# Kernel optimization log

Hardware: AMD Instinct MI355X
Metric: run time of the kernel (lower is better)

The kernel has to match this reference:

```python
import jax, jax.numpy as jnp
import numpy as np
from jax import lax

CLAMP = 4.135
OUT = 7            # RoI pool output size
SCALE = 1.0 / 16.0 # feature-map stride 16


def bilinear_gather(feat, bidx, y, x):
    """feat [B,C,H,W]; bidx [N] int; y,x [N,Ph,Pw] coords in feature space -> [N,C,Ph,Pw]."""
    B, C, H, W = feat.shape
    y = jnp.clip(y, 0.0, H - 1.0)
    x = jnp.clip(x, 0.0, W - 1.0)
    y0 = jnp.floor(y); x0 = jnp.floor(x)
    y0i = y0.astype(jnp.int32); x0i = x0.astype(jnp.int32)
    y1i = jnp.minimum(y0i + 1, H - 1); x1i = jnp.minimum(x0i + 1, W - 1)
    wy1 = y - y0; wx1 = x - x0
    wy0 = 1.0 - wy1; wx0 = 1.0 - wx1
    flat = feat.transpose(0, 2, 3, 1).reshape(B * H * W, C)
    base = (bidx * (H * W))[:, None, None]
    def g(yy, xx):
        return flat[base + yy * W + xx]  # [N,Ph,Pw,C]
    out = ((wy0 * wx0)[..., None] * g(y0i, x0i)
           + (wy0 * wx1)[..., None] * g(y0i, x1i)
           + (wy1 * wx0)[..., None] * g(y1i, x0i)
           + (wy1 * wx1)[..., None] * g(y1i, x1i))
    return out.transpose(0, 3, 1, 2)


def roi_align(feat, boxes, bidx):
    """RoIAlign, sampling_ratio=1 (one bilinear sample per bin center)."""
    N = boxes.shape[0]
    b = boxes * SCALE
    x1, y1, x2, y2 = b[:, 0], b[:, 1], b[:, 2], b[:, 3]
    bw = jnp.maximum(x2 - x1, 1.0) / OUT
    bh = jnp.maximum(y2 - y1, 1.0) / OUT
    c = jnp.arange(OUT, dtype=feat.dtype) + 0.5
    ys = y1[:, None] + c * bh[:, None]   # [N,OUT]
    xs = x1[:, None] + c * bw[:, None]
    yg = jnp.broadcast_to(ys[:, :, None], (N, OUT, OUT))
    xg = jnp.broadcast_to(xs[:, None, :], (N, OUT, OUT))
    return bilinear_gather(feat, bidx, yg, xg)


def xyxy_to_rbox(b):
    cx = (b[:, 0] + b[:, 2]) * 0.5
    cy = (b[:, 1] + b[:, 3]) * 0.5
    w = b[:, 2] - b[:, 0]
    h = b[:, 3] - b[:, 1]
    return jnp.stack([cx, cy, w, h, jnp.zeros_like(cx)], axis=1)


def decode_deltas_to_rboxes(rboxes, deltas):
    cx, cy, w, h, a = (rboxes[:, i] for i in range(5))
    dx, dy, dw, dh, da = (deltas[:, i] for i in range(5))
    return jnp.stack([cx + dx * w, cy + dy * h,
                      w * jnp.exp(dw), h * jnp.exp(dh), a + da], axis=1)


def grid_sample_zeros(feat, gx, gy):
    """F.grid_sample(bilinear, padding_mode='zeros', align_corners=False).
    feat [N,C,H,W]; gx,gy [N,Ho,Wo] normalized coords -> [N,C,Ho,Wo]."""
    N, C, H, W = feat.shape
    ix = ((gx + 1.0) * W - 1.0) * 0.5
    iy = ((gy + 1.0) * H - 1.0) * 0.5
    x0 = jnp.floor(ix); y0 = jnp.floor(iy)
    wx1 = ix - x0; wy1 = iy - y0
    x0i = x0.astype(jnp.int32); y0i = y0.astype(jnp.int32)
    flat = feat.transpose(0, 2, 3, 1).reshape(N, H * W, C)
    Ho, Wo = gx.shape[1], gx.shape[2]
    def g(yy, xx, wt):
        valid = ((yy >= 0) & (yy < H) & (xx >= 0) & (xx < W)).astype(feat.dtype)
        idx = jnp.clip(yy, 0, H - 1) * W + jnp.clip(xx, 0, W - 1)
        v = jnp.take_along_axis(flat, idx.reshape(N, -1, 1), axis=1)
        v = v.reshape(N, Ho, Wo, C)
        return (wt * valid)[..., None] * v
    out = (g(y0i, x0i, (1 - wy1) * (1 - wx1))
           + g(y0i, x0i + 1, (1 - wy1) * wx1)
           + g(y0i + 1, x0i, wy1 * (1 - wx1))
           + g(y0i + 1, x0i + 1, wy1 * wx1))
    return out.transpose(0, 3, 1, 2)


def setup_inputs() -> dict:
    key = jax.random.key(0)
    ks = jax.random.split(key, 12)
    B, C, H, W = 2, 256, 64, 64
    N, NC = 2048, 16
    FD = C * OUT * OUT  # 12544
    features = jax.random.normal(ks[0], (B, C, H, W), jnp.float32)
    # valid image-space boxes (image 1024x1024, stride-16 features)
    cx = jax.random.uniform(ks[1], (N,), minval=96.0, maxval=928.0)
    cy = jax.random.uniform(ks[2], (N,), minval=96.0, maxval=928.0)
    bw = jax.random.uniform(ks[3], (N,), minval=16.0, maxval=128.0)
    bh = jax.random.uniform(ks[4], (N,), minval=16.0, maxval=128.0)
    proposals = jnp.stack([cx - bw / 2, cy - bh / 2, cx + bw / 2, cy + bh / 2], axis=1)
    batch_idx = jnp.repeat(jnp.arange(B, dtype=jnp.int32), N // B)
    s = 0.02
    return {
        "features": features,
        "proposals": proposals,
        "batch_idx": batch_idx,
        "conv_w": jax.random.normal(ks[5], (C, C, 3, 3), jnp.float32) * s,
        "conv_b": jnp.zeros((C,), jnp.float32),
        "align_w": jax.random.normal(ks[6], (5, FD), jnp.float32) * s,
        "align_b": jnp.zeros((5,), jnp.float32),
        "fc1_w": jax.random.normal(ks[7], (1024, FD), jnp.float32) * s,
        "fc1_b": jnp.zeros((1024,), jnp.float32),
        "fc2_w": jax.random.normal(ks[8], (1024, 1024), jnp.float32) * s,
        "fc2_b": jnp.zeros((1024,), jnp.float32),
        "cls_w": jax.random.normal(ks[9], (NC, 1024), jnp.float32) * s,
        "cls_b": jnp.zeros((NC,), jnp.float32),
        "box_w": jax.random.normal(ks[10], (5, 1024), jnp.float32) * s,
        "box_b": jnp.zeros((5,), jnp.float32),
    }


def reference(features, proposals, batch_idx, conv_w, conv_b, align_w, align_b,
              fc1_w, fc1_b, fc2_w, fc2_b, cls_w, cls_b, box_w, box_b):
    N = proposals.shape[0]
    # 1) RoI align
    box_feat = roi_align(features, proposals, batch_idx)           # [N,256,7,7]
    a = lax.conv_general_dilated(box_feat, conv_w, (1, 1), ((1, 1), (1, 1)),
                                 dimension_numbers=("NCHW", "OIHW", "NCHW"))
    a = jax.nn.relu(a + conv_b[None, :, None, None]).reshape(N, -1)
    coarse = jnp.clip(a @ align_w.T + align_b, -CLAMP, CLAMP)      # [N,5]
    # 3) decode to rboxes (torch.no_grad -> stop_gradient)
    prop_rb = xyxy_to_rbox(proposals)
    align_rb = lax.stop_gradient(decode_deltas_to_rboxes(prop_rb, coarse))
    # 4) affine grid from rbox (no translation, matches source) + grid_sample
    w, h, ang = align_rb[:, 2], align_rb[:, 3], align_rb[:, 4]
    cth, sth = jnp.cos(ang), jnp.sin(ang)
    sx, sy = w / OUT, h / OUT
    base = (2.0 * jnp.arange(OUT, dtype=box_feat.dtype) + 1.0) / OUT - 1.0
    xb = base[None, None, :]
    yb = base[None, :, None]
    gx = (sx * cth)[:, None, None] * xb + (-(sy * sth))[:, None, None] * yb
    gy = (sx * sth)[:, None, None] * xb + (sy * cth)[:, None, None] * yb
    aligned = grid_sample_zeros(box_feat, gx, gy)                  # [N,256,7,7]
    # 5) refine head MLP + predictors
    r = jax.nn.relu(aligned.reshape(N, -1) @ fc1_w.T + fc1_b)
    r = jax.nn.relu(r @ fc2_w.T + fc2_b)
    logits = r @ cls_w.T + cls_b                                   # [N,16]
    final = jnp.clip(r @ box_w.T + box_b, -CLAMP, CLAMP)           # [N,5]
    # 6) eval-path decode + softmax (per-class NMS is dynamic-shape postproc, excluded)
    pred_rboxes = decode_deltas_to_rboxes(prop_rb, final)
    scores = jax.nn.softmax(logits, axis=-1)
    return jnp.concatenate([pred_rboxes, scores], axis=1)          # [N,21]
```

## Files before the change

kernel.cpp:

```cpp
#include <hip/hip_runtime.h>
#include <hip/hip_bf16.h>
#include <math.h>
#include <type_traits>

constexpr int B = 2, C = 256, H = 64, W = 64, HW = H * W;
constexpr int N = 2048, OUT = 7, P = 49, FD = C * P;
constexpr int K1 = 1024;
constexpr float CLAMP_V = 4.135f, SCALE_V = 1.0f / 16.0f;
constexpr int LDB = 264;

typedef short s8v __attribute__((ext_vector_type(8)));
typedef short s4v __attribute__((ext_vector_type(4)));
typedef float f32x4 __attribute__((ext_vector_type(4)));

template <int I, int NN, class F>
__device__ __forceinline__ void static_for(F&& f) {
    if constexpr (I < NN) {
        f(std::integral_constant<int, I>{});
        static_for<I + 1, NN>(static_cast<F&&>(f));
    }
}

__device__ __forceinline__ int xcd_swz(int blk, int nblk) {
    const int cpx = nblk >> 3;
    return (blk & 7) * cpx + (blk >> 3);
}

__global__ void k_transpose_feat(const float* __restrict__ in, float* __restrict__ out) {
    __shared__ float tile[32][33];
    const int b  = blockIdx.z;
    const int c0 = blockIdx.y * 32;
    const int p0 = blockIdx.x * 32;
    const int tx = threadIdx.x % 32, ty = threadIdx.x / 32;
#pragma unroll
    for (int r = 0; r < 32; r += 8)
        tile[ty + r][tx] = in[(size_t)(b * C + c0 + ty + r) * HW + p0 + tx];
    __syncthreads();
#pragma unroll
    for (int r = 0; r < 32; r += 8)
        out[(size_t)(b * HW + p0 + ty + r) * C + c0 + tx] = tile[tx][ty + r];
}

__global__ void k_prep_wB(const float* __restrict__ in, __hip_bfloat16* __restrict__ out) {
    const int T = blockIdx.x;
    const int tap = T / 8, s = T % 8;
    const int co = threadIdx.x;
#pragma unroll
    for (int q = 0; q < 4; ++q)
#pragma unroll
        for (int j = 0; j < 8; ++j) {
            const int ci = s * 32 + q * 8 + j;
            out[(((size_t)T * 256 + co) * 4 + q) * 8 + j] =
                __float2bfloat16(in[(size_t)co * 2304 + ci * 9 + tap]);
        }
}

__global__ void k_prep_aw(const float* __restrict__ in, float4* __restrict__ out4,
                          float* __restrict__ out1) {
    const int o = blockIdx.x;
    const int co = threadIdx.x;
    float4 v;
    v.x = in[(size_t)0 * FD + co * 49 + o];
    v.y = in[(size_t)1 * FD + co * 49 + o];
    v.z = in[(size_t)2 * FD + co * 49 + o];
    v.w = in[(size_t)3 * FD + co * 49 + o];
    out4[o * 256 + co] = v;
    out1[o * 256 + co] = in[(size_t)4 * FD + co * 49 + o];
}

__global__ void k_f2b(const float* __restrict__ in, __hip_bfloat16* __restrict__ out, int n4) {
    for (int i = blockIdx.x * blockDim.x + threadIdx.x; i < n4; i += gridDim.x * blockDim.x) {
        const float4 v = reinterpret_cast<const float4*>(in)[i];
        out[i * 4 + 0] = __float2bfloat16(v.x);
        out[i * 4 + 1] = __float2bfloat16(v.y);
        out[i * 4 + 2] = __float2bfloat16(v.z);
        out[i * 4 + 3] = __float2bfloat16(v.w);
    }
}

__global__ void k_prep_fc1(const float* __restrict__ in, __hip_bfloat16* __restrict__ out) {
    __shared__ float lds[64 * 49];
    const int o  = blockIdx.y;
    const int c0 = blockIdx.x * 64;
    const int t  = threadIdx.x;
    const float* src = in + (size_t)o * FD + (size_t)c0 * 49;
    for (int i = t; i < 64 * 49; i += 256) lds[i] = src[i];
    __syncthreads();
    __hip_bfloat16* dst = out + (size_t)o * FD + c0;
    for (int j = t; j < 64 * 49; j += 256) {
        const int p = j >> 6, cc = j & 63;
        dst[(size_t)p * 256 + cc] = __float2bfloat16(lds[cc * 49 + p]);
    }
}

__global__ __launch_bounds__(256, 2) void k_roi_conv_grid(
    const float* __restrict__ featT, const float* __restrict__ proposals,
    const int* __restrict__ bidx, const __hip_bfloat16* __restrict__ wB,
    const float* __restrict__ conv_b, const float4* __restrict__ aw4,
    const float* __restrict__ aw1, const float* __restrict__ align_b,
    __hip_bfloat16* __restrict__ alignedOut) {
    __shared__ __align__(16) __hip_bfloat16 bfh[2][50 * LDB];
    __shared__ float red[64];

    const int blk = xcd_swz(blockIdx.x, 1024);
    const int t = threadIdx.x;
    const int lane = t & 63, wid = t >> 6;
    const int l15 = lane & 15;
    const int qofs = (lane >> 4) * 8;

#pragma unroll
    for (int r = 0; r < 2; ++r) {
        const int n = blk * 2 + r;
        const float px1 = proposals[n * 4 + 0] * SCALE_V, py1 = proposals[n * 4 + 1] * SCALE_V;
        const float px2 = proposals[n * 4 + 2] * SCALE_V, py2 = proposals[n * 4 + 3] * SCALE_V;
        const float bw = fmaxf(px2 - px1, 1.0f) * (1.0f / OUT);
        const float bh = fmaxf(py2 - py1, 1.0f) * (1.0f / OUT);
        const int b = bidx[n];
        const float* fb = featT + (size_t)b * HW * C;
        for (int p = wid; p < P; p += 4) {
            const int pyi = p / 7, pxi = p % 7;
            float y = py1 + (pyi + 0.5f) * bh;
            float x = px1 + (pxi + 0.5f) * bw;
            y = fminf(fmaxf(y, 0.f), (float)(H - 1));
            x = fminf(fmaxf(x, 0.f), (float)(W - 1));
            const float y0f = floorf(y), x0f = floorf(x);
            const int y0 = (int)y0f, x0 = (int)x0f;
            const int y1 = min(y0 + 1, H - 1), x1 = min(x0 + 1, W - 1);
            const float wy1 = y - y0f, wx1 = x - x0f;
            const float wy0 = 1.f - wy1, wx0 = 1.f - wx1;
            const int c4 = lane * 4;
            const float4 v00 = *reinterpret_cast<const float4*>(&fb[(size_t)(y0 * W + x0) * C + c4]);
            const float4 v01 = *reinterpret_cast<const float4*>(&fb[(size_t)(y0 * W + x1) * C + c4]);
            const float4 v10 = *reinterpret_cast<const float4*>(&fb[(size_t)(y1 * W + x0) * C + c4]);
            const float4 v11 = *reinterpret_cast<const float4*>(&fb[(size_t)(y1 * W + x1) * C + c4]);
            s4v o4;
            o4[0] = (short)__bfloat16_as_ushort(__float2bfloat16(
                        wy0 * (wx0 * v00.x + wx1 * v01.x) + wy1 * (wx0 * v10.x + wx1 * v11.x)));
            o4[1] = (short)__bfloat16_as_ushort(__float2bfloat16(
                        wy0 * (wx0 * v00.y + wx1 * v01.y) + wy1 * (wx0 * v10.y + wx1 * v11.y)));
            o4[2] = (short)__bfloat16_as_ushort(__float2bfloat16(
                        wy0 * (wx0 * v00.z + wx1 * v01.z) + wy1 * (wx0 * v10.z + wx1 * v11.z)));
            o4[3] = (short)__bfloat16_as_ushort(__float2bfloat16(
                        wy0 * (wx0 * v00.w + wx1 * v01.w) + wy1 * (wx0 * v10.w + wx1 * v11.w)));
            *reinterpret_cast<s4v*>(&bfh[r][p * LDB + c4]) = o4;
        }
        bfh[r][49 * LDB + t] = __float2bfloat16(0.f);
    }
    __syncthreads();

    int oyt[4], oxt[4];
    static_for<0, 4>([&](auto MT) {
        const int o = MT.value * 16 + l15;
        oyt[MT.value] = o / 7;
        oxt[MT.value] = o % 7;
    });
    int bofs[4];
    static_for<0, 4>([&](auto NT) {
        const int col = wid * 64 + NT.value * 16 + l15;
        bofs[NT.value] = col * 32 + qofs;
    });

    f32x4 acc[2][4][4] = {};
    for (int tap = 0; tap < 9; ++tap) {
        const int dy = tap / 3 - 1, dx = tap % 3 - 1;
        int rsel[4];
        static_for<0, 4>([&](auto MT) {
            const int iy = oyt[MT.value] + dy, ix = oxt[MT.value] + dx;
            const bool v = ((unsigned)iy < 7u) && ((unsigned)ix < 7u);
            rsel[MT.value] = (v ? (iy * 7 + ix) : 49) * LDB;
        });
        const __hip_bfloat16* wTap = wB + (size_t)tap * 8 * 8192;
#pragma unroll
        for (int s = 0; s < 8; ++s) {
            s8v af[2][4], bfr[4];
            static_for<0, 4>([&](auto NT) {
                bfr[NT.value] = *reinterpret_cast<const s8v*>(&wTap[(size_t)s * 8192 + bofs[NT.value]]);
            });
            static_for<0, 2>([&](auto RI) {
                static_for<0, 4>([&](auto MT) {
                    af[RI.value][MT.value] = *reinterpret_cast<const s8v*>(
                        &bfh[RI.value][rsel[MT.value] + s * 32 + qofs]);
                });
            });
            __builtin_amdgcn_s_setprio(1);
            static_for<0, 2>([&](auto RI) {
                static_for<0, 4>([&](auto MT) {
                    static_for<0, 4>([&](auto NT) {
                        acc[RI.value][MT.value][NT.value] = __builtin_amdgcn_mfma_f32_16x16x32_bf16(
                            af[RI.value][MT.value], bfr[NT.value],
                            acc[RI.value][MT.value][NT.value], 0, 0, 0);
                    });
                });
            });
            __builtin_amdgcn_s_setprio(0);
        }
    }

    float cb[4];
    static_for<0, 4>([&](auto NT) { cb[NT.value] = conv_b[wid * 64 + NT.value * 16 + l15]; });
    float pc[2][5] = {};
    static_for<0, 4>([&](auto MT) {
        static_for<0, 4>([&](auto RR) {
            const int o = MT.value * 16 + (lane >> 4) * 4 + RR.value;
            if (o < 49) {
                static_for<0, 4>([&](auto NT) {
                    const int co = wid * 64 + NT.value * 16 + l15;
                    const float4 w4 = aw4[o * 256 + co];
                    const float  w1 = aw1[o * 256 + co];
                    static_for<0, 2>([&](auto RI) {
                        const float a = fmaxf(acc[RI.value][MT.value][NT.value][RR.value] + cb[NT.value], 0.f);
                        pc[RI.value][0] = fmaf(a, w4.x, pc[RI.value][0]);
                        pc[RI.value][1] = fmaf(a, w4.y, pc[RI.value][1]);
                        pc[RI.value][2] = fmaf(a, w4.z, pc[RI.value][2]);
                        pc[RI.value][3] = fmaf(a, w4.w, pc[RI.value][3]);
                        pc[RI.value][4] = fmaf(a, w1,   pc[RI.value][4]);
                    });
                });
            }
        });
    });
    static_for<0, 2>([&](auto RI) {
        static_for<0, 5>([&](auto J) {
            float s = pc[RI.value][J.value];
#pragma unroll
            for (int off = 32; off; off >>= 1) s += __shfl_xor(s, off);
            pc[RI.value][J.value] = s;
        });
        if (lane == 0) {
            static_for<0, 5>([&](auto J) { red[RI.value * 20 + wid * 5 + J.value] = pc[RI.value][J.value]; });
        }
    });
    __syncthreads();

    if (t < 2) {
        const int r = t;
        const int n = blk * 2 + r;
        float coarse[5];
        static_for<0, 5>([&](auto Jc) {
            constexpr int j = Jc.value;
            float s = red[r * 20 + j] + red[r * 20 + 5 + j] + red[r * 20 + 10 + j] +
                      red[r * 20 + 15 + j] + align_b[j];
            coarse[j] = fminf(fmaxf(s, -CLAMP_V), CLAMP_V);
        });
        const float x1r = proposals[n * 4 + 0], y1r = proposals[n * 4 + 1];
        const float x2r = proposals[n * 4 + 2], y2r = proposals[n * 4 + 3];
        const float w = x2r - x1r, h = y2r - y1r;
        const float w2 = w * expf(coarse[2]);
        const float h2 = h * expf(coarse[3]);
        const float ang = coarse[4];
        const float cth = cosf(ang), sth = sinf(ang);
        const float sx = w2 * (1.0f / OUT), sy = h2 * (1.0f / OUT);
        red[48 + r * 4 + 0] = sx * cth;
        red[48 + r * 4 + 1] = sy * sth;
        red[48 + r * 4 + 2] = sx * sth;
        red[48 + r * 4 + 3] = sy * cth;
    }
    __syncthreads();

#pragma unroll
    for (int r = 0; r < 2; ++r) {
        const float gA = red[48 + r * 4 + 0], gBv = red[48 + r * 4 + 1];
        const float gC = red[48 + r * 4 + 2], gD = red[48 + r * 4 + 3];
        const __hip_bfloat16* bh = bfh[r];
        __hip_bfloat16* ao = alignedOut + (size_t)(blk * 2 + r) * FD;
        for (int p = 0; p < P; ++p) {
            const int pyi = p / 7, pxi = p % 7;
            const float xb = (2 * pxi + 1) * (1.0f / OUT) - 1.0f;
            const float yb = (2 * pyi + 1) * (1.0f / OUT) - 1.0f;
            const float gx = gA * xb - gBv * yb;
            const float gy = gC * xb + gD * yb;
            const float ix = ((gx + 1.0f) * OUT - 1.0f) * 0.5f;
            const float iy = ((gy + 1.0f) * OUT - 1.0f) * 0.5f;
            const float x0f = floorf(ix), y0f = floorf(iy);
            const int x0 = (int)x0f, y0 = (int)y0f;
            const float wx1 = ix - x0f, wy1 = iy - y0f;
            const float wx0 = 1.f - wx1, wy0 = 1.f - wy1;
            const bool vx0 = (unsigned)x0 < 7u, vx1 = (unsigned)(x0 + 1) < 7u;
            const bool vy0 = (unsigned)y0 < 7u, vy1 = (unsigned)(y0 + 1) < 7u;
            const int r00 = (vy0 && vx0) ? (y0 * 7 + x0) : 49;
            const int r01 = (vy0 && vx1) ? (y0 * 7 + x0 + 1) : 49;
            const int r10 = (vy1 && vx0) ? ((y0 + 1) * 7 + x0) : 49;
            const int r11 = (vy1 && vx1) ? ((y0 + 1) * 7 + x0 + 1) : 49;
            float val;
            val  = (wy0 * wx0) * __bfloat162float(bh[r00 * LDB + t]);
            val += (wy0 * wx1) * __bfloat162float(bh[r01 * LDB + t]);
            val += (wy1 * wx0) * __bfloat162float(bh[r10 * LDB + t]);
            val += (wy1 * wx1) * __bfloat162float(bh[r11 * LDB + t]);
            ao[p * 256 + t] = __float2bfloat16(val);
        }
    }
}

template <int BM, int BN, int BK>
__global__ __launch_bounds__(256, 4) void k_gemm_bf16(
    const __hip_bfloat16* __restrict__ A, const __hip_bfloat16* __restrict__ Wt,
    const float* __restrict__ bias, float* __restrict__ CoutF,
    __hip_bfloat16* __restrict__ CoutH, int M, int Nn, int K, int relu) {
    constexpr int LD = BK + 8;
    __shared__ __align__(16) __hip_bfloat16 As[2][BM * LD];
    __shared__ __align__(16) __hip_bfloat16 Ws[2][BN * LD];
    const int ntb = Nn / BN;
    const int blkS = xcd_swz(blockIdx.x, gridDim.x);
    const int bx = blkS % ntb, by = blkS / ntb;
    const int t = threadIdx.x;
    const int lane = t & 63, wid = t >> 6;
    const int l15 = lane & 15;
    const int qofs = (lane >> 4) * 8;
    const int wm = wid >> 1, wn = wid & 1;

    const int ar = t >> 3, ak = (t & 7) * 8;
    const size_t aBase = (size_t)(by * BM) * K;
    const size_t bBase = (size_t)(bx * BN) * K;

    f32x4 acc[2][2] = {};

    const int steps = K / BK;
    {
        const s8v a0 = *reinterpret_cast<const s8v*>(&A[aBase + (size_t)ar * K + ak]);
        const s8v a1 = *reinterpret_cast<const s8v*>(&A[aBase + (size_t)(ar + 32) * K + ak]);
        const s8v b0 = *reinterpret_cast<const s8v*>(&Wt[bBase + (size_t)ar * K + ak]);
        const s8v b1 = *reinterpret_cast<const s8v*>(&Wt[bBase + (size_t)(ar + 32) * K + ak]);
        *reinterpret_cast<s8v*>(&As[0][ar * LD + ak]) = a0;
        *reinterpret_cast<s8v*>(&As[0][(ar + 32) * LD + ak]) = a1;
        *reinterpret_cast<s8v*>(&Ws[0][ar * LD + ak]) = b0;
        *reinterpret_cast<s8v*>(&Ws[0][(ar + 32) * LD + ak]) = b1;
    }
    __syncthreads();

    for (int s = 0; s < steps; ++s) {
        const int cur = s & 1;
        const bool pf = (s + 1 < steps);
        s8v a0, a1, b0, b1;
        if (pf) {
            const int k0 = (s + 1) * BK;
            a0 = *reinterpret_cast<const s8v*>(&A[aBase + (size_t)ar * K + k0 + ak]);
            a1 = *reinterpret_cast<const s8v*>(&A[aBase + (size_t)(ar + 32) * K + k0 + ak]);
            b0 = *reinterpret_cast<const s8v*>(&Wt[bBase + (size_t)ar * K + k0 + ak]);
            b1 = *reinterpret_cast<const s8v*>(&Wt[bBase + (size_t)(ar + 32) * K + k0 + ak]);
        }
        static_for<0, 2>([&](auto KH) {
            s8v afr[2], bfr[2];
            static_for<0, 2>([&](auto MT) {
                afr[MT.value] = *reinterpret_cast<const s8v*>(
                    &As[cur][(wm * 32 + MT.value * 16 + l15) * LD + KH.value * 32 + qofs]);
            });
            static_for<0, 2>([&](auto NT) {
                bfr[NT.value] = *reinterpret_cast<const s8v*>(
                    &Ws[cur][(wn * 32 + NT.value * 16 + l15) * LD + KH.value * 32 + qofs]);
            });
            static_for<0, 2>([&](auto MT) {
                static_for<0, 2>([&](auto NT) {
                    acc[MT.value][NT.value] = __builtin_amdgcn_mfma_f32_16x16x32_bf16(
                        afr[MT.value], bfr[NT.value], acc[MT.value][NT.value], 0, 0, 0);
                });
            });
        });
        if (pf) {
            __syncthreads();
            const int nxt = cur ^ 1;
            *reinterpret_cast<s8v*>(&As[nxt][ar * LD + ak]) = a0;
            *reinterpret_cast<s8v*>(&As[nxt][(ar + 32) * LD + ak]) = a1;
            *reinterpret_cast<s8v*>(&Ws[nxt][ar * LD + ak]) = b0;
            *reinterpret_cast<s8v*>(&Ws[nxt][(ar + 32) * LD + ak]) = b1;
            __syncthreads();
        }
    }

    static_for<0, 2>([&](auto MT) {
        static_for<0, 2>([&](auto NT) {
            const int col = bx * BN + wn * 32 + NT.value * 16 + l15;
            const float bv = bias[col];
            static_for<0, 4>([&](auto RR) {
                const int row = by * BM + wm * 32 + MT.value * 16 + (lane >> 4) * 4 + RR.value;
                float v = acc[MT.value][NT.value][RR.value] + bv;
                if (relu) v = fmaxf(v, 0.f);
                if (CoutF) CoutF[(size_t)row * Nn + col] = v;
                if (CoutH) CoutH[(size_t)row * Nn + col] = __float2bfloat16(v);
            });
        });
    });
}

__global__ void k_heads(const float* __restrict__ r2, const float* __restrict__ cls_w,
                        const float* __restrict__ cls_b, const float* __restrict__ box_w,
                        const float* __restrict__ box_b, const float* __restrict__ proposals,
                        float* __restrict__ out) {
    const int n = blockIdx.x;
    const int t = threadIdx.x;
    const float* r = r2 + (size_t)n * K1;
    float rv[16];
    static_for<0, 16>([&](auto Jc) { rv[Jc.value] = r[t + 64 * Jc.value]; });
    float s[21];
    static_for<0, 21>([&](auto Oc) {
        constexpr int o = Oc.value;
        const float* w = (o < 16) ? (cls_w + (size_t)o * K1) : (box_w + (size_t)(o - 16) * K1);
        float a = 0.f;
        static_for<0, 16>([&](auto Jc) { a = fmaf(rv[Jc.value], w[t + 64 * Jc.value], a); });
#pragma unroll
        for (int off = 32; off; off >>= 1) a += __shfl_xor(a, off);
        s[o] = a;
    });
    float logits[16];
    float m = -1e30f;
    static_for<0, 16>([&](auto Oc) {
        logits[Oc.value] = s[Oc.value] + cls_b[Oc.value];
        m = fmaxf(m, logits[Oc.value]);
    });
    float es = 0.f;
    static_for<0, 16>([&](auto Oc) {
        logits[Oc.value] = expf(logits[Oc.value] - m);
        es += logits[Oc.value];
    });
    const float inv = 1.0f / es;
    float fdelta[5];
    static_for<0, 5>([&](auto Jc) {
        fdelta[Jc.value] = fminf(fmaxf(s[16 + Jc.value] + box_b[Jc.value], -CLAMP_V), CLAMP_V);
    });
    const float x1r = proposals[n * 4 + 0], y1r = proposals[n * 4 + 1];
    const float x2r = proposals[n * 4 + 2], y2r = proposals[n * 4 + 3];
    const float cx = (x1r + x2r) * 0.5f, cy = (y1r + y2r) * 0.5f;
    const float w = x2r - x1r, h = y2r - y1r;
    float pred[5];
    pred[0] = cx + fdelta[0] * w;
    pred[1] = cy + fdelta[1] * h;
    pred[2] = w * expf(fdelta[2]);
    pred[3] = h * expf(fdelta[3]);
    pred[4] = fdelta[4];
    float* orow = out + (size_t)n * 21;
    static_for<0, 5>([&](auto Oc) {
        if (t == Oc.value) orow[Oc.value] = pred[Oc.value];
    });
    static_for<0, 16>([&](auto Oc) {
        if (t == 5 + Oc.value) orow[5 + Oc.value] = logits[Oc.value] * inv;
    });
}

extern "C" void kernel_launch(void* const* d_in, const int* in_sizes, int n_in,
                              void* d_out, int out_size, void* d_ws, size_t ws_size,
                              hipStream_t stream) {
    (void)in_sizes; (void)n_in; (void)out_size; (void)ws_size;
    const float* features  = (const float*)d_in[0];
    const float* proposals = (const float*)d_in[1];
    const int*   batch_idx = (const int*)d_in[2];
    const float* conv_w    = (const float*)d_in[3];
    const float* conv_b    = (const float*)d_in[4];
    const float* align_w   = (const float*)d_in[5];
    const float* align_b   = (const float*)d_in[6];
    const float* fc1_w     = (const float*)d_in[7];
    const float* fc1_b     = (const float*)d_in[8];
    const float* fc2_w     = (const float*)d_in[9];
    const float* fc2_b     = (const float*)d_in[10];
    const float* cls_w     = (const float*)d_in[11];
    const float* cls_b     = (const float*)d_in[12];
    const float* box_w     = (const float*)d_in[13];
    const float* box_b     = (const float*)d_in[14];
    float* out = (float*)d_out;

    float* ws    = (float*)d_ws;
    float* featT = ws;
    float* r2    = featT + (size_t)B * HW * C;
    float4* aw4  = (float4*)(r2 + (size_t)N * K1);
    float* aw1   = (float*)(aw4 + 49 * 256);
    __hip_bfloat16* alignedH = (__hip_bfloat16*)(aw1 + 49 * 256);
    __hip_bfloat16* r1H   = alignedH + (size_t)N * FD;
    __hip_bfloat16* wB    = r1H + (size_t)N * K1;
    __hip_bfloat16* fc1B  = wB + 2304 * 256;
    __hip_bfloat16* fc2B  = fc1B + (size_t)K1 * FD;

    k_transpose_feat<<<dim3(HW / 32, C / 32, B), 256, 0, stream>>>(features, featT);
    k_prep_wB<<<72, 256, 0, stream>>>(conv_w, wB);
    k_prep_aw<<<49, 256, 0, stream>>>(align_w, aw4, aw1);
    k_prep_fc1<<<dim3(4, K1), 256, 0, stream>>>(fc1_w, fc1B);
    k_f2b<<<256, 256, 0, stream>>>(fc2_w, fc2B, (K1 * K1) / 4);
    k_roi_conv_grid<<<N / 2, 256, 0, stream>>>(featT, proposals, batch_idx, wB, conv_b,
                                               aw4, aw1, align_b, alignedH);
    k_gemm_bf16<64, 64, 64><<<(N / 64) * (K1 / 64), 256, 0, stream>>>(
        alignedH, fc1B, fc1_b, nullptr, r1H, N, K1, FD, 1);
    k_gemm_bf16<64, 64, 64><<<(N / 64) * (K1 / 64), 256, 0, stream>>>(
        r1H, fc2B, fc2_b, r2, nullptr, N, K1, K1, 1);
    k_heads<<<N, 64, 0, stream>>>(r2, cls_w, cls_b, box_w, box_b, proposals, out);
}
```

Baseline: 355.5 us.

## Interleave two RoIs in conv M dimension and fuse prep kernels into one launch

Merges the five weight/feature preparation kernels into a single launch dispatched by block index, removing per-launch overhead and letting the small prep jobs run concurrently. In the RoI conv kernel, the two RoIs' bilinear samples are interleaved row-wise in LDS so the 98 valid rows form a single M dimension of 7 MFMA tiles instead of 2×4 tiles with padding. This cuts wasted MFMA work on padded rows (128 to 112 rows per tap) and the A-fragment loads. It trades this for more complex row indexing in the epilogue and grid-sample stages.

```diff
diff --git a/kernel.cpp b/kernel.cpp
--- a/kernel.cpp
+++ b/kernel.cpp
@@ -26,70 +26,71 @@
     return (blk & 7) * cpx + (blk >> 3);
 }
 
-__global__ void k_transpose_feat(const float* __restrict__ in, float* __restrict__ out) {
-    __shared__ float tile[32][33];
-    const int b  = blockIdx.z;
-    const int c0 = blockIdx.y * 32;
-    const int p0 = blockIdx.x * 32;
-    const int tx = threadIdx.x % 32, ty = threadIdx.x / 32;
-#pragma unroll
-    for (int r = 0; r < 32; r += 8)
-        tile[ty + r][tx] = in[(size_t)(b * C + c0 + ty + r) * HW + p0 + tx];
-    __syncthreads();
-#pragma unroll
-    for (int r = 0; r < 32; r += 8)
-        out[(size_t)(b * HW + p0 + ty + r) * C + c0 + tx] = tile[tx][ty + r];
-}
-
-__global__ void k_prep_wB(const float* __restrict__ in, __hip_bfloat16* __restrict__ out) {
-    const int T = blockIdx.x;
-    const int tap = T / 8, s = T % 8;
-    const int co = threadIdx.x;
-#pragma unroll
-    for (int q = 0; q < 4; ++q)
-#pragma unroll
-        for (int j = 0; j < 8; ++j) {
-            const int ci = s * 32 + q * 8 + j;
-            out[(((size_t)T * 256 + co) * 4 + q) * 8 + j] =
-                __float2bfloat16(in[(size_t)co * 2304 + ci * 9 + tap]);
-        }
-}
-
-__global__ void k_prep_aw(const float* __restrict__ in, float4* __restrict__ out4,
-                          float* __restrict__ out1) {
-    const int o = blockIdx.x;
-    const int co = threadIdx.x;
-    float4 v;
-    v.x = in[(size_t)0 * FD + co * 49 + o];
-    v.y = in[(size_t)1 * FD + co * 49 + o];
-    v.z = in[(size_t)2 * FD + co * 49 + o];
-    v.w = in[(size_t)3 * FD + co * 49 + o];
-    out4[o * 256 + co] = v;
-    out1[o * 256 + co] = in[(size_t)4 * FD + co * 49 + o];
-}
-
-__global__ void k_f2b(const float* __restrict__ in, __hip_bfloat16* __restrict__ out, int n4) {
-    for (int i = blockIdx.x * blockDim.x + threadIdx.x; i < n4; i += gridDim.x * blockDim.x) {
-        const float4 v = reinterpret_cast<const float4*>(in)[i];
-        out[i * 4 + 0] = __float2bfloat16(v.x);
-        out[i * 4 + 1] = __float2bfloat16(v.y);
-        out[i * 4 + 2] = __float2bfloat16(v.z);
-        out[i * 4 + 3] = __float2bfloat16(v.w);
-    }
-}
-
-__global__ void k_prep_fc1(const float* __restrict__ in, __hip_bfloat16* __restrict__ out) {
-    __shared__ float lds[64 * 49];
-    const int o  = blockIdx.y;
-    const int c0 = blockIdx.x * 64;
-    const int t  = threadIdx.x;
-    const float* src = in + (size_t)o * FD + (size_t)c0 * 49;
-    for (int i = t; i < 64 * 49; i += 256) lds[i] = src[i];
-    __syncthreads();
-    __hip_bfloat16* dst = out + (size_t)o * FD + c0;
-    for (int j = t; j < 64 * 49; j += 256) {
-        const int p = j >> 6, cc = j & 63;
-        dst[(size_t)p * 256 + cc] = __float2bfloat16(lds[cc * 49 + p]);
+__global__ void k_prep_all(const float* __restrict__ features, float* __restrict__ featT,
+                           const float* __restrict__ conv_w, __hip_bfloat16* __restrict__ wB,
+                           const float* __restrict__ align_w, float4* __restrict__ aw4,
+                           float* __restrict__ aw1,
+                           const float* __restrict__ fc1_w, __hip_bfloat16* __restrict__ fc1B,
+                           const float* __restrict__ fc2_w, __hip_bfloat16* __restrict__ fc2B) {
+    __shared__ float smem[64 * 49];
+    const int id = blockIdx.x;
+    const int t = threadIdx.x;
+    if (id < 2048) {
+        const int x = id % 128, y = (id / 128) % 8, b = id / 1024;
+        const int c0 = y * 32, p0 = x * 32;
+        const int tx = t % 32, ty = t / 32;
+        float* tile = smem;
+#pragma unroll
+        for (int r = 0; r < 32; r += 8)
+            tile[(ty + r) * 33 + tx] = features[(size_t)(b * C + c0 + ty + r) * HW + p0 + tx];
+        __syncthreads();
+#pragma unroll
+        for (int r = 0; r < 32; r += 8)
+            featT[(size_t)(b * HW + p0 + ty + r) * C + c0 + tx] = tile[tx * 33 + ty + r];
+    } else if (id < 2120) {
+        const int T = id - 2048;
+        const int tap = T / 8, s = T % 8;
+        const int co = t;
+#pragma unroll
+        for (int q = 0; q < 4; ++q)
+#pragma unroll
+            for (int j = 0; j < 8; ++j) {
+                const int ci = s * 32 + q * 8 + j;
+                wB[(((size_t)T * 256 + co) * 4 + q) * 8 + j] =
+                    __float2bfloat16(conv_w[(size_t)co * 2304 + ci * 9 + tap]);
+            }
+    } else if (id < 2169) {
+        const int o = id - 2120;
+        const int co = t;
+        float4 v;
+        v.x = align_w[(size_t)0 * FD + co * 49 + o];
+        v.y = align_w[(size_t)1 * FD + co * 49 + o];
+        v.z = align_w[(size_t)2 * FD + co * 49 + o];
+        v.w = align_w[(size_t)3 * FD + co * 49 + o];
+        aw4[o * 256 + co] = v;
+        aw1[o * 256 + co] = align_w[(size_t)4 * FD + co * 49 + o];
+    } else if (id < 6265) {
+        const int q = id - 2169;
+        const int c0 = (q % 4) * 64;
+        const int o = q / 4;
+        const float* src = fc1_w + (size_t)o * FD + (size_t)c0 * 49;
+        for (int i = t; i < 64 * 49; i += 256) smem[i] = src[i];
+        __syncthreads();
+        __hip_bfloat16* dst = fc1B + (size_t)o * FD + c0;
+        for (int j = t; j < 64 * 49; j += 256) {
+            const int p = j >> 6, cc = j & 63;
+            dst[(size_t)p * 256 + cc] = __float2bfloat16(smem[cc * 49 + p]);
+        }
+    } else {
+        const int bid = id - 6265;
+        const int n4 = (K1 * K1) / 4;
+        for (int i = bid * 256 + t; i < n4; i += 256 * 256) {
+            const float4 v = reinterpret_cast<const float4*>(fc2_w)[i];
+            fc2B[i * 4 + 0] = __float2bfloat16(v.x);
+            fc2B[i * 4 + 1] = __float2bfloat16(v.y);
+            fc2B[i * 4 + 2] = __float2bfloat16(v.z);
+            fc2B[i * 4 + 3] = __float2bfloat16(v.w);
+        }
     }
 }
 
@@ -99,7 +100,7 @@
     const float* __restrict__ conv_b, const float4* __restrict__ aw4,
     const float* __restrict__ aw1, const float* __restrict__ align_b,
     __hip_bfloat16* __restrict__ alignedOut) {
-    __shared__ __align__(16) __hip_bfloat16 bfh[2][50 * LDB];
+    __shared__ __align__(16) __hip_bfloat16 bfh[100 * LDB];
     __shared__ float red[64];
 
     const int blk = xcd_swz(blockIdx.x, 1024);
@@ -142,17 +143,21 @@
                         wy0 * (wx0 * v00.z + wx1 * v01.z) + wy1 * (wx0 * v10.z + wx1 * v11.z)));
             o4[3] = (short)__bfloat16_as_ushort(__float2bfloat16(
                         wy0 * (wx0 * v00.w + wx1 * v01.w) + wy1 * (wx0 * v10.w + wx1 * v11.w)));
-            *reinterpret_cast<s4v*>(&bfh[r][p * LDB + c4]) = o4;
-        }
-        bfh[r][49 * LDB + t] = __float2bfloat16(0.f);
-    }
+            *reinterpret_cast<s4v*>(&bfh[(2 * p + r) * LDB + c4]) = o4;
+        }
+    }
+    bfh[98 * LDB + t] = __float2bfloat16(0.f);
+    bfh[99 * LDB + t] = __float2bfloat16(0.f);
     __syncthreads();
 
-    int oyt[4], oxt[4];
-    static_for<0, 4>([&](auto MT) {
-        const int o = MT.value * 16 + l15;
-        oyt[MT.value] = o / 7;
-        oxt[MT.value] = o % 7;
+    const int rp = l15 & 1;
+    int oyt[7], oxt[7];
+    bool pval[7];
+    static_for<0, 7>([&](auto MT) {
+        const int p = (MT.value * 16 + l15) >> 1;
+        pval[MT.value] = (p < 49);
+        oyt[MT.value] = p / 7;
+        oxt[MT.value] = p % 7;
     });
     int bofs[4];
     static_for<0, 4>([&](auto NT) {
@@ -160,61 +165,55 @@
         bofs[NT.value] = col * 32 + qofs;
     });
 
-    f32x4 acc[2][4][4] = {};
+    f32x4 acc[7][4] = {};
     for (int tap = 0; tap < 9; ++tap) {
         const int dy = tap / 3 - 1, dx = tap % 3 - 1;
-        int rsel[4];
-        static_for<0, 4>([&](auto MT) {
+        int rsel[7];
+        static_for<0, 7>([&](auto MT) {
             const int iy = oyt[MT.value] + dy, ix = oxt[MT.value] + dx;
-            const bool v = ((unsigned)iy < 7u) && ((unsigned)ix < 7u);
-            rsel[MT.value] = (v ? (iy * 7 + ix) : 49) * LDB;
+            const bool v = pval[MT.value] && ((unsigned)iy < 7u) && ((unsigned)ix < 7u);
+            rsel[MT.value] = (v ? (2 * (iy * 7 + ix) + rp) : (98 + rp)) * LDB;
         });
         const __hip_bfloat16* wTap = wB + (size_t)tap * 8 * 8192;
 #pragma unroll
         for (int s = 0; s < 8; ++s) {
-            s8v af[2][4], bfr[4];
+            s8v af[7], bfr[4];
             static_for<0, 4>([&](auto NT) {
                 bfr[NT.value] = *reinterpret_cast<const s8v*>(&wTap[(size_t)s * 8192 + bofs[NT.value]]);
             });
-            static_for<0, 2>([&](auto RI) {
-                static_for<0, 4>([&](auto MT) {
-                    af[RI.value][MT.value] = *reinterpret_cast<const s8v*>(
-                        &bfh[RI.value][rsel[MT.value] + s * 32 + qofs]);
+            static_for<0, 7>([&](auto MT) {
+                af[MT.value] = *reinterpret_cast<const s8v*>(&bfh[rsel[MT.value] + s * 32 + qofs]);
+            });
+            __builtin_amdgcn_s_setprio(1);
+            static_for<0, 7>([&](auto MT) {
+                static_for<0, 4>([&](auto NT) {
+                    acc[MT.value][NT.value] = __builtin_amdgcn_mfma_f32_16x16x32_bf16(
+                        af[MT.value], bfr[NT.value], acc[MT.value][NT.value], 0, 0, 0);
                 });
             });
-            __builtin_amdgcn_s_setprio(1);
-            static_for<0, 2>([&](auto RI) {
-                static_for<0, 4>([&](auto MT) {
-                    static_for<0, 4>([&](auto NT) {
-                        acc[RI.value][MT.value][NT.value] = __builtin_amdgcn_mfma_f32_16x16x32_bf16(
-                            af[RI.value][MT.value], bfr[NT.value],
-                            acc[RI.value][MT.value][NT.value], 0, 0, 0);
-                    });
-                });
-            });
             __builtin_amdgcn_s_setprio(0);
         }
     }
 
+    const int hi = lane >> 4;
     float cb[4];
     static_for<0, 4>([&](auto NT) { cb[NT.value] = conv_b[wid * 64 + NT.value * 16 + l15]; });
     float pc[2][5] = {};
-    static_for<0, 4>([&](auto MT) {
+    static_for<0, 7>([&](auto MT) {
         static_for<0, 4>([&](auto RR) {
-            const int o = MT.value * 16 + (lane >> 4) * 4 + RR.value;
-            if (o < 49) {
+            constexpr int r = RR.value & 1;
+            const int p = MT.value * 8 + hi * 2 + (RR.value >> 1);
+            if (p < 49) {
                 static_for<0, 4>([&](auto NT) {
                     const int co = wid * 64 + NT.value * 16 + l15;
-                    const float4 w4 = aw4[o * 256 + co];
-                    const float  w1 = aw1[o * 256 + co];
-                    static_for<0, 2>([&](auto RI) {
-                        const float a = fmaxf(acc[RI.value][MT.value][NT.value][RR.value] + cb[NT.value], 0.f);
-                        pc[RI.value][0] = fmaf(a, w4.x, pc[RI.value][0]);
-                        pc[RI.value][1] = fmaf(a, w4.y, pc[RI.value][1]);
-                        pc[RI.value][2] = fmaf(a, w4.z, pc[RI.value][2]);
-                        pc[RI.value][3] = fmaf(a, w4.w, pc[RI.value][3]);
-                        pc[RI.value][4] = fmaf(a, w1,   pc[RI.value][4]);
-                    });
+                    const float4 w4 = aw4[p * 256 + co];
+                    const float  w1 = aw1[p * 256 + co];
+                    const float a = fmaxf(acc[MT.value][NT.value][RR.value] + cb[NT.value], 0.f);
+                    pc[r][0] = fmaf(a, w4.x, pc[r][0]);
+                    pc[r][1] = fmaf(a, w4.y, pc[r][1]);
+                    pc[r][2] = fmaf(a, w4.z, pc[r][2]);
+                    pc[r][3] = fmaf(a, w4.w, pc[r][3]);
+                    pc[r][4] = fmaf(a, w1,   pc[r][4]);
                 });
             }
         });
@@ -261,7 +260,6 @@
     for (int r = 0; r < 2; ++r) {
         const float gA = red[48 + r * 4 + 0], gBv = red[48 + r * 4 + 1];
         const float gC = red[48 + r * 4 + 2], gD = red[48 + r * 4 + 3];
-        const __hip_bfloat16* bh = bfh[r];
         __hip_bfloat16* ao = alignedOut + (size_t)(blk * 2 + r) * FD;
         for (int p = 0; p < P; ++p) {
             const int pyi = p / 7, pxi = p % 7;
@@ -282,10 +280,10 @@
             const int r10 = (vy1 && vx0) ? ((y0 + 1) * 7 + x0) : 49;
             const int r11 = (vy1 && vx1) ? ((y0 + 1) * 7 + x0 + 1) : 49;
             float val;
-            val  = (wy0 * wx0) * __bfloat162float(bh[r00 * LDB + t]);
-            val += (wy0 * wx1) * __bfloat162float(bh[r01 * LDB + t]);
-            val += (wy1 * wx0) * __bfloat162float(bh[r10 * LDB + t]);
-            val += (wy1 * wx1) * __bfloat162float(bh[r11 * LDB + t]);
+            val  = (wy0 * wx0) * __bfloat162float(bfh[(2 * r00 + r) * LDB + t]);
+            val += (wy0 * wx1) * __bfloat162float(bfh[(2 * r01 + r) * LDB + t]);
+            val += (wy1 * wx0) * __bfloat162float(bfh[(2 * r10 + r) * LDB + t]);
+            val += (wy1 * wx1) * __bfloat162float(bfh[(2 * r11 + r) * LDB + t]);
             ao[p * 256 + t] = __float2bfloat16(val);
         }
     }
@@ -467,11 +465,8 @@
     __hip_bfloat16* fc1B  = wB + 2304 * 256;
     __hip_bfloat16* fc2B  = fc1B + (size_t)K1 * FD;
 
-    k_transpose_feat<<<dim3(HW / 32, C / 32, B), 256, 0, stream>>>(features, featT);
-    k_prep_wB<<<72, 256, 0, stream>>>(conv_w, wB);
-    k_prep_aw<<<49, 256, 0, stream>>>(align_w, aw4, aw1);
-    k_prep_fc1<<<dim3(4, K1), 256, 0, stream>>>(fc1_w, fc1B);
-    k_f2b<<<256, 256, 0, stream>>>(fc2_w, fc2B, (K1 * K1) / 4);
+    k_prep_all<<<6521, 256, 0, stream>>>(features, featT, conv_w, wB, align_w, aw4, aw1,
+                                         fc1_w, fc1B, fc2_w, fc2B);
     k_roi_conv_grid<<<N / 2, 256, 0, stream>>>(featT, proposals, batch_idx, wB, conv_b,
                                                aw4, aw1, align_b, alignedH);
     k_gemm_bf16<64, 64, 64><<<(N / 64) * (K1 / 64), 256, 0, stream>>>(
```

Result: faster. 336.6 us (-5.3%).
